# Optimization experiments

Measured on AMD Instinct MI355X. Metric: run time of the kernel, lower is better.

## Reference

```python
import jax, jax.numpy as jnp
import numpy as np

N = 100000
E = 1600000
IN_DIM = 128
OUT_DIM = 128


def setup_inputs() -> dict:
    key = jax.random.key(0)
    k1, k2, k3, k4, k5 = jax.random.split(key, 5)
    x = jax.random.normal(k1, (N, IN_DIM), dtype=jnp.float32)
    edge_index = jax.random.randint(k2, (2, E), 0, N, dtype=jnp.int64)
    # LayerNorm affine params
    ln_w = jnp.ones((IN_DIM,), dtype=jnp.float32)
    ln_b = jnp.zeros((IN_DIM,), dtype=jnp.float32)
    # SAGEConv params: lin_l (neighbor agg, with bias), lin_r (root, no bias)
    s = 1.0 / np.sqrt(IN_DIM)
    W_l = jax.random.uniform(k3, (OUT_DIM, IN_DIM), dtype=jnp.float32, minval=-s, maxval=s)
    b_l = jax.random.uniform(k4, (OUT_DIM,), dtype=jnp.float32, minval=-s, maxval=s)
    W_r = jax.random.uniform(k5, (OUT_DIM, IN_DIM), dtype=jnp.float32, minval=-s, maxval=s)
    return {"x": x, "edge_index": edge_index, "ln_w": ln_w, "ln_b": ln_b,
            "W_l": W_l, "b_l": b_l, "W_r": W_r}


def _layer_norm(x, w, b, eps=1e-5):
    mu = jnp.mean(x, axis=-1, keepdims=True)
    var = jnp.mean(jnp.square(x - mu), axis=-1, keepdims=True)
    return (x - mu) * jax.lax.rsqrt(var + eps) * w + b


def reference(x, edge_index, ln_w, ln_b, W_l, b_l, W_r):
    # norm -> activation -> dropout(p=0, identity)
    h = jax.nn.relu(_layer_norm(x, ln_w, ln_b))  # [N, in_dim]
    src = edge_index[0]  # message sources (x_j)
    dst = edge_index[1]  # aggregation targets
    # mean aggregation of neighbor features onto target nodes
    agg = jax.ops.segment_sum(h[src], dst, num_segments=N)  # [N, in_dim]
    cnt = jax.ops.segment_sum(jnp.ones((E,), dtype=h.dtype), dst, num_segments=N)
    agg = agg / jnp.maximum(cnt, 1.0)[:, None]
    # SAGEConv: lin_l(agg) + lin_r(h)
    out = agg @ W_l.T + b_l + h @ W_r.T  # [N, out_dim]
    return out
```

## Files before the change

kernel.cpp:

```cpp
#include <hip/hip_runtime.h>

#define N_NODES 100000
#define E_EDGES 1600000
#define DIM     128

#define NB1     391
#define NBINS   512
#define NBH     (NBINS * NB1)
#define HS_BLOCKS 196

#define HB_OFF    0
#define AGGB_OFF  25600000
#define WTB_OFF   51200000
#define OFFS_OFF  51265536
#define BH_OFF    51665600
#define BSUM_OFF  52468416
#define BIN_OFF   52469440

typedef __attribute__((ext_vector_type(8))) short short8;
typedef __attribute__((ext_vector_type(4))) float floatx4;

__device__ __forceinline__ unsigned bf16pack(float a, float b) {
  unsigned ua = __float_as_uint(a); ua += 0x7fffu + ((ua >> 16) & 1u);
  unsigned ub = __float_as_uint(b); ub += 0x7fffu + ((ub >> 16) & 1u);
  return (ua >> 16) | (ub & 0xffff0000u);
}
__device__ __forceinline__ float2 bf16unpack(unsigned p) {
  return make_float2(__uint_as_float(p << 16), __uint_as_float(p & 0xffff0000u));
}

__global__ __launch_bounds__(256) void k_prep(const float* __restrict__ x,
                                              const float* __restrict__ lw,
                                              const float* __restrict__ lb,
                                              const float* __restrict__ Wl,
                                              const float* __restrict__ Wr,
                                              unsigned* __restrict__ hb,
                                              unsigned* __restrict__ wtb) {
  int gid = blockIdx.x * 256 + threadIdx.x;

  {
    int row  = blockIdx.x * 4 + (threadIdx.x >> 6);
    int lane = threadIdx.x & 63;
    float2 v = ((const float2*)(x + (size_t)row * DIM))[lane];
    float s  = v.x + v.y;
    float sq = v.x * v.x + v.y * v.y;
    #pragma unroll
    for (int off = 32; off > 0; off >>= 1) {
      s  += __shfl_xor(s, off);
      sq += __shfl_xor(sq, off);
    }
    float mu  = s * (1.0f / 128.0f);
    float var = sq * (1.0f / 128.0f) - mu * mu;
    float rs  = rsqrtf(var + 1e-5f);
    float2 w = ((const float2*)lw)[lane];
    float2 b = ((const float2*)lb)[lane];
    float ox = fmaxf((v.x - mu) * rs * w.x + b.x, 0.0f);
    float oy = fmaxf((v.y - mu) * rs * w.y + b.y, 0.0f);
    hb[(size_t)row * 64 + lane] = bf16pack(ox, oy);
  }

  if (gid < 16384) {
    int j2 = gid & 3;
    int q  = (gid >> 2) & 3;
    int c  = (gid >> 4) & 127;
    int kb = gid >> 11;
    int k0 = kb * 32 + q * 8 + j2 * 2;
    int k1 = k0 + 1;
    float v0 = (k0 < 128) ? Wl[c * 128 + k0] : Wr[c * 128 + (k0 - 128)];
    float v1 = (k1 < 128) ? Wl[c * 128 + k1] : Wr[c * 128 + (k1 - 128)];
    wtb[gid] = bf16pack(v0, v1);
  }
}

__global__ __launch_bounds__(256) void k_hist1(const int* __restrict__ ei,
                                               int* __restrict__ bh) {
  __shared__ int h[NBINS];
  int t = threadIdx.x;
  h[t] = 0; h[t + 256] = 0;
  __syncthreads();
  const int4* d4p = (const int4*)(ei + E_EDGES);
  #pragma unroll
  for (int u = 0; u < 4; ++u) {
    int i4 = blockIdx.x * 1024 + u * 256 + t;
    if (i4 < E_EDGES / 4) {
      int4 d = d4p[i4];
      atomicAdd(&h[d.x >> 8], 1);
      atomicAdd(&h[d.y >> 8], 1);
      atomicAdd(&h[d.z >> 8], 1);
      atomicAdd(&h[d.w >> 8], 1);
    }
  }
  __syncthreads();
  bh[t * NB1 + blockIdx.x] = h[t];
  bh[(t + 256) * NB1 + blockIdx.x] = h[t + 256];
}

__global__ __launch_bounds__(256) void k_hscan1(int* __restrict__ bh,
                                                int* __restrict__ bsum) {
  __shared__ int s[256];
  int t = threadIdx.x;
  int base = blockIdx.x * 1024 + t * 4;
  int a0 = (base + 0 < NBH) ? bh[base + 0] : 0;
  int a1 = (base + 1 < NBH) ? bh[base + 1] : 0;
  int a2 = (base + 2 < NBH) ? bh[base + 2] : 0;
  int a3 = (base + 3 < NBH) ? bh[base + 3] : 0;
  s[t] = a0 + a1 + a2 + a3;
  __syncthreads();
  #pragma unroll
  for (int off = 1; off < 256; off <<= 1) {
    int x = (t >= off) ? s[t - off] : 0;
    __syncthreads();
    s[t] += x;
    __syncthreads();
  }
  int excl = (t > 0) ? s[t - 1] : 0;
  if (t == 255) bsum[blockIdx.x] = s[255];
  if (base + 0 < NBH) bh[base + 0] = excl;
  if (base + 1 < NBH) bh[base + 1] = excl + a0;
  if (base + 2 < NBH) bh[base + 2] = excl + a0 + a1;
  if (base + 3 < NBH) bh[base + 3] = excl + a0 + a1 + a2;
}

__global__ __launch_bounds__(256) void k_hscan2(int* __restrict__ bh,
                                                const int* __restrict__ bsum) {
  __shared__ int s[256];
  int t = threadIdx.x;
  s[t] = (t < HS_BLOCKS) ? bsum[t] : 0;
  __syncthreads();
  #pragma unroll
  for (int off = 1; off < 256; off <<= 1) {
    int x = (t >= off) ? s[t - off] : 0;
    __syncthreads();
    s[t] += x;
    __syncthreads();
  }
  int blk = blockIdx.x;
  int add = (blk > 0) ? s[blk - 1] : 0;
  #pragma unroll
  for (int u = 0; u < 4; ++u) {
    int i = blk * 1024 + t * 4 + u;
    if (i < NBH) bh[i] += add;
  }
}

__global__ __launch_bounds__(256) void k_scatter1(const int* __restrict__ ei,
                                                  const int* __restrict__ bh,
                                                  int* __restrict__ binned) {
  __shared__ int cur[NBINS];
  int t = threadIdx.x;
  cur[t] = bh[t * NB1 + blockIdx.x];
  cur[t + 256] = bh[(t + 256) * NB1 + blockIdx.x];
  __syncthreads();
  const int4* s4p = (const int4*)ei;
  const int4* d4p = (const int4*)(ei + E_EDGES);
  #pragma unroll
  for (int u = 0; u < 4; ++u) {
    int i4 = blockIdx.x * 1024 + u * 256 + t;
    if (i4 < E_EDGES / 4) {
      int4 sv = s4p[i4];
      int4 dv = d4p[i4];
      int p0 = atomicAdd(&cur[dv.x >> 8], 1);
      int p1 = atomicAdd(&cur[dv.y >> 8], 1);
      int p2 = atomicAdd(&cur[dv.z >> 8], 1);
      int p3 = atomicAdd(&cur[dv.w >> 8], 1);
      binned[p0] = sv.x | ((dv.x & 255) << 20);
      binned[p1] = sv.y | ((dv.y & 255) << 20);
      binned[p2] = sv.z | ((dv.z & 255) << 20);
      binned[p3] = sv.w | ((dv.w & 255) << 20);
    }
  }
}

__global__ __launch_bounds__(256) void k_csr(const int* __restrict__ bh,
                                             const int* __restrict__ binned,
                                             int* __restrict__ offs,
                                             int* __restrict__ srcidx) {
  __shared__ int h[256];
  __shared__ int s[256];
  __shared__ int cur[256];
  int t = threadIdx.x;
  int bin = blockIdx.x;
  int base = bh[bin * NB1];
  int end  = bh[(bin + 1) * NB1];
  h[t] = 0;
  __syncthreads();
  for (int i = base + t; i < end; i += 256)
    atomicAdd(&h[(binned[i] >> 20) & 255], 1);
  __syncthreads();
  s[t] = h[t];
  __syncthreads();
  #pragma unroll
  for (int off = 1; off < 256; off <<= 1) {
    int x = (t >= off) ? s[t - off] : 0;
    __syncthreads();
    s[t] += x;
    __syncthreads();
  }
  int excl = (t > 0) ? s[t - 1] : 0;
  cur[t] = excl;
  int node = bin * 256 + t;
  if (node < N_NODES) offs[node] = base + excl;
  if (node == N_NODES) offs[N_NODES] = E_EDGES;
  __syncthreads();
  for (int i = base + t; i < end; i += 256) {
    int p = binned[i];
    int r = atomicAdd(&cur[(p >> 20) & 255], 1);
    srcidx[base + r] = p & 0xFFFFF;
  }
}

__global__ __launch_bounds__(256) void k_gather(const unsigned* __restrict__ hb,
                                                const int* __restrict__ offs,
                                                const int* __restrict__ srcidx,
                                                unsigned* __restrict__ aggb) {
  int wave = threadIdx.x >> 6;
  int lane = threadIdx.x & 63;
  int n0 = blockIdx.x * 8 + wave * 2;
  int n1 = n0 + 1;
  int b0 = __builtin_amdgcn_readfirstlane(offs[n0]);
  int e0 = __builtin_amdgcn_readfirstlane(offs[n0 + 1]);
  int b1 = __builtin_amdgcn_readfirstlane(offs[n1]);
  int e1 = __builtin_amdgcn_readfirstlane(offs[n1 + 1]);
  int m0 = e0 - b0, m1 = e1 - b1;
  int c  = (m0 < m1 ? m0 : m1) & ~7;

  float ax0 = 0.0f, ay0 = 0.0f, ax1 = 0.0f, ay1 = 0.0f;

  for (int j = 0; j < c; j += 8) {
    unsigned p0[8], p1[8];
    #pragma unroll
    for (int i = 0; i < 8; ++i) {
      int s0 = srcidx[b0 + j + i];
      int s1 = srcidx[b1 + j + i];
      p0[i] = hb[(size_t)s0 * 64 + lane];
      p1[i] = hb[(size_t)s1 * 64 + lane];
    }
    #pragma unroll
    for (int i = 0; i < 8; ++i) {
      float2 v0 = bf16unpack(p0[i]);
      float2 v1 = bf16unpack(p1[i]);
      ax0 += v0.x; ay0 += v0.y;
      ax1 += v1.x; ay1 += v1.y;
    }
  }
  for (int j = b0 + c; j < e0; ) {
    int rem = e0 - j;
    if (rem >= 8) {
      unsigned p[8];
      #pragma unroll
      for (int i = 0; i < 8; ++i) p[i] = hb[(size_t)srcidx[j + i] * 64 + lane];
      #pragma unroll
      for (int i = 0; i < 8; ++i) { float2 v = bf16unpack(p[i]); ax0 += v.x; ay0 += v.y; }
      j += 8;
    } else {
      float2 v = bf16unpack(hb[(size_t)srcidx[j] * 64 + lane]);
      ax0 += v.x; ay0 += v.y;
      ++j;
    }
  }
  for (int j = b1 + c; j < e1; ) {
    int rem = e1 - j;
    if (rem >= 8) {
      unsigned p[8];
      #pragma unroll
      for (int i = 0; i < 8; ++i) p[i] = hb[(size_t)srcidx[j + i] * 64 + lane];
      #pragma unroll
      for (int i = 0; i < 8; ++i) { float2 v = bf16unpack(p[i]); ax1 += v.x; ay1 += v.y; }
      j += 8;
    } else {
      float2 v = bf16unpack(hb[(size_t)srcidx[j] * 64 + lane]);
      ax1 += v.x; ay1 += v.y;
      ++j;
    }
  }

  float inv0 = 1.0f / fmaxf((float)m0, 1.0f);
  float inv1 = 1.0f / fmaxf((float)m1, 1.0f);
  aggb[(size_t)n0 * 64 + lane] = bf16pack(ax0 * inv0, ay0 * inv0);
  aggb[(size_t)n1 * 64 + lane] = bf16pack(ax1 * inv1, ay1 * inv1);
}

__global__ __launch_bounds__(256) void k_gemm(const unsigned* __restrict__ aggb,
                                              const unsigned* __restrict__ hb,
                                              const unsigned* __restrict__ wtb,
                                              const float* __restrict__ bl,
                                              float* __restrict__ out) {
  int wave = threadIdx.x >> 6;
  int lane = threadIdx.x & 63;
  int m = lane & 15;
  int q = lane >> 4;
  int r0 = blockIdx.x * 64 + wave * 16;
  int rowA = r0 + m;
  if (rowA > N_NODES - 1) rowA = N_NODES - 1;

  const uint4* ar = (const uint4*)(aggb + (size_t)rowA * 64);
  const uint4* hr = (const uint4*)(hb + (size_t)rowA * 64);
  short8 afrag[8];
  #pragma unroll
  for (int kb = 0; kb < 4; ++kb) {
    uint4 u = ar[kb * 4 + q];
    afrag[kb] = *(short8*)&u;
  }
  #pragma unroll
  for (int kb = 0; kb < 4; ++kb) {
    uint4 u = hr[kb * 4 + q];
    afrag[kb + 4] = *(short8*)&u;
  }

  const uint4* b4 = (const uint4*)wtb;
  #pragma unroll
  for (int ct = 0; ct < 8; ++ct) {
    int c = ct * 16 + m;
    floatx4 acc = {0.0f, 0.0f, 0.0f, 0.0f};
    #pragma unroll
    for (int kb = 0; kb < 8; ++kb) {
      uint4 u = b4[kb * 512 + c * 4 + q];
      short8 bfrag = *(short8*)&u;
      acc = __builtin_amdgcn_mfma_f32_16x16x32_bf16(afrag[kb], bfrag, acc, 0, 0, 0);
    }
    float bias = bl[c];
    #pragma unroll
    for (int reg = 0; reg < 4; ++reg) {
      int r = r0 + q * 4 + reg;
      if (r < N_NODES) out[(size_t)r * DIM + c] = acc[reg] + bias;
    }
  }
}

extern "C" void kernel_launch(void* const* d_in, const int* in_sizes, int n_in,
                              void* d_out, int out_size, void* d_ws, size_t ws_size,
                              hipStream_t stream) {
  const float* x  = (const float*)d_in[0];
  const int*   ei = (const int*)d_in[1];
  const float* lw = (const float*)d_in[2];
  const float* lb = (const float*)d_in[3];
  const float* Wl = (const float*)d_in[4];
  const float* bl = (const float*)d_in[5];
  const float* Wr = (const float*)d_in[6];
  float* out = (float*)d_out;

  char* ws = (char*)d_ws;
  unsigned* hb     = (unsigned*)(ws + HB_OFF);
  unsigned* aggb   = (unsigned*)(ws + AGGB_OFF);
  unsigned* wtb    = (unsigned*)(ws + WTB_OFF);
  int*      offs   = (int*)(ws + OFFS_OFF);
  int*      bh     = (int*)(ws + BH_OFF);
  int*      bsum   = (int*)(ws + BSUM_OFF);
  int*      binned = (int*)(ws + BIN_OFF);
  int*      srcidx = binned;
  srcidx = (int*)(ws + BIN_OFF);

  srcidx = (int*)(ws + BIN_OFF + (size_t)E_EDGES * 4);

  k_prep<<<N_NODES / 4, 256, 0, stream>>>(x, lw, lb, Wl, Wr, hb, wtb);
  k_hist1<<<NB1, 256, 0, stream>>>(ei, bh);
  k_hscan1<<<HS_BLOCKS, 256, 0, stream>>>(bh, bsum);
  k_hscan2<<<HS_BLOCKS, 256, 0, stream>>>(bh, bsum);
  k_scatter1<<<NB1, 256, 0, stream>>>(ei, bh, binned);
  k_csr<<<NB1, 256, 0, stream>>>(bh, binned, offs, srcidx);
  k_gather<<<N_NODES / 8, 256, 0, stream>>>(hb, offs, srcidx, aggb);
  k_gemm<<<(N_NODES + 63) / 64, 256, 0, stream>>>(aggb, hb, wtb, bl, out);
}
```

Baseline: 265.8 us.

## Fuse all stages into one persistent cooperative kernel with grid syncs

Replaces the eight separate kernel launches with a single persistent cooperative kernel. Its blocks grid-stride over each former stage, and grid.sync() separates the stages. This removes per-launch overhead and inter-kernel gaps. In exchange, occupancy is capped by the cooperative grid size and launch bounds, the whole grid waits at every barrier, and large stages like the gather now run with fewer resident blocks.

```diff
diff --git a/kernel.cpp b/kernel.cpp
--- a/kernel.cpp
+++ b/kernel.cpp
@@ -1,4 +1,7 @@
 #include <hip/hip_runtime.h>
+#include <hip/hip_cooperative_groups.h>
+
+namespace cg = cooperative_groups;
 
 #define N_NODES 100000
 #define E_EDGES 1600000
@@ -16,6 +19,7 @@
 #define BH_OFF    51665600
 #define BSUM_OFF  52468416
 #define BIN_OFF   52469440
+#define SRC_OFF   58869440
 
 typedef __attribute__((ext_vector_type(8))) short short8;
 typedef __attribute__((ext_vector_type(4))) float floatx4;
@@ -29,28 +33,41 @@
   return make_float2(__uint_as_float(p << 16), __uint_as_float(p & 0xffff0000u));
 }
 
-__global__ __launch_bounds__(256) void k_prep(const float* __restrict__ x,
-                                              const float* __restrict__ lw,
-                                              const float* __restrict__ lb,
-                                              const float* __restrict__ Wl,
-                                              const float* __restrict__ Wr,
-                                              unsigned* __restrict__ hb,
-                                              unsigned* __restrict__ wtb) {
-  int gid = blockIdx.x * 256 + threadIdx.x;
-
-  {
-    int row  = blockIdx.x * 4 + (threadIdx.x >> 6);
-    int lane = threadIdx.x & 63;
+__global__ __launch_bounds__(256, 4) void k_mega(
+    const float* __restrict__ x, const int* __restrict__ ei,
+    const float* __restrict__ lw, const float* __restrict__ lb,
+    const float* __restrict__ Wl, const float* __restrict__ bl,
+    const float* __restrict__ Wr, float* __restrict__ out,
+    char* __restrict__ ws) {
+  unsigned* hb     = (unsigned*)(ws + HB_OFF);
+  unsigned* aggb   = (unsigned*)(ws + AGGB_OFF);
+  unsigned* wtb    = (unsigned*)(ws + WTB_OFF);
+  int*      offs   = (int*)(ws + OFFS_OFF);
+  int*      bh     = (int*)(ws + BH_OFF);
+  int*      bsum   = (int*)(ws + BSUM_OFF);
+  int*      binned = (int*)(ws + BIN_OFF);
+  int*      srcidx = (int*)(ws + SRC_OFF);
+
+  cg::grid_group grid = cg::this_grid();
+  __shared__ int smem[768];
+  const int t    = threadIdx.x;
+  const int blk  = blockIdx.x;
+  const int gdim = gridDim.x;
+  const int lane = t & 63;
+  const int wv   = t >> 6;
+
+  for (int g = blk; g < N_NODES / 4; g += gdim) {
+    int row = g * 4 + wv;
     float2 v = ((const float2*)(x + (size_t)row * DIM))[lane];
-    float s  = v.x + v.y;
-    float sq = v.x * v.x + v.y * v.y;
+    float sAcc = v.x + v.y;
+    float qAcc = v.x * v.x + v.y * v.y;
     #pragma unroll
     for (int off = 32; off > 0; off >>= 1) {
-      s  += __shfl_xor(s, off);
-      sq += __shfl_xor(sq, off);
-    }
-    float mu  = s * (1.0f / 128.0f);
-    float var = sq * (1.0f / 128.0f) - mu * mu;
+      sAcc += __shfl_xor(sAcc, off);
+      qAcc += __shfl_xor(qAcc, off);
+    }
+    float mu  = sAcc * (1.0f / 128.0f);
+    float var = qAcc * (1.0f / 128.0f) - mu * mu;
     float rs  = rsqrtf(var + 1e-5f);
     float2 w = ((const float2*)lw)[lane];
     float2 b = ((const float2*)lb)[lane];
@@ -58,271 +75,251 @@
     float oy = fmaxf((v.y - mu) * rs * w.y + b.y, 0.0f);
     hb[(size_t)row * 64 + lane] = bf16pack(ox, oy);
   }
-
-  if (gid < 16384) {
-    int j2 = gid & 3;
-    int q  = (gid >> 2) & 3;
-    int c  = (gid >> 4) & 127;
-    int kb = gid >> 11;
-    int k0 = kb * 32 + q * 8 + j2 * 2;
-    int k1 = k0 + 1;
-    float v0 = (k0 < 128) ? Wl[c * 128 + k0] : Wr[c * 128 + (k0 - 128)];
-    float v1 = (k1 < 128) ? Wl[c * 128 + k1] : Wr[c * 128 + (k1 - 128)];
-    wtb[gid] = bf16pack(v0, v1);
-  }
-}
-
-__global__ __launch_bounds__(256) void k_hist1(const int* __restrict__ ei,
-                                               int* __restrict__ bh) {
-  __shared__ int h[NBINS];
-  int t = threadIdx.x;
-  h[t] = 0; h[t + 256] = 0;
-  __syncthreads();
-  const int4* d4p = (const int4*)(ei + E_EDGES);
-  #pragma unroll
-  for (int u = 0; u < 4; ++u) {
-    int i4 = blockIdx.x * 1024 + u * 256 + t;
-    if (i4 < E_EDGES / 4) {
-      int4 d = d4p[i4];
-      atomicAdd(&h[d.x >> 8], 1);
-      atomicAdd(&h[d.y >> 8], 1);
-      atomicAdd(&h[d.z >> 8], 1);
-      atomicAdd(&h[d.w >> 8], 1);
-    }
-  }
-  __syncthreads();
-  bh[t * NB1 + blockIdx.x] = h[t];
-  bh[(t + 256) * NB1 + blockIdx.x] = h[t + 256];
-}
-
-__global__ __launch_bounds__(256) void k_hscan1(int* __restrict__ bh,
-                                                int* __restrict__ bsum) {
-  __shared__ int s[256];
-  int t = threadIdx.x;
-  int base = blockIdx.x * 1024 + t * 4;
-  int a0 = (base + 0 < NBH) ? bh[base + 0] : 0;
-  int a1 = (base + 1 < NBH) ? bh[base + 1] : 0;
-  int a2 = (base + 2 < NBH) ? bh[base + 2] : 0;
-  int a3 = (base + 3 < NBH) ? bh[base + 3] : 0;
-  s[t] = a0 + a1 + a2 + a3;
-  __syncthreads();
-  #pragma unroll
-  for (int off = 1; off < 256; off <<= 1) {
-    int x = (t >= off) ? s[t - off] : 0;
-    __syncthreads();
-    s[t] += x;
-    __syncthreads();
-  }
-  int excl = (t > 0) ? s[t - 1] : 0;
-  if (t == 255) bsum[blockIdx.x] = s[255];
-  if (base + 0 < NBH) bh[base + 0] = excl;
-  if (base + 1 < NBH) bh[base + 1] = excl + a0;
-  if (base + 2 < NBH) bh[base + 2] = excl + a0 + a1;
-  if (base + 3 < NBH) bh[base + 3] = excl + a0 + a1 + a2;
-}
-
-__global__ __launch_bounds__(256) void k_hscan2(int* __restrict__ bh,
-                                                const int* __restrict__ bsum) {
-  __shared__ int s[256];
-  int t = threadIdx.x;
-  s[t] = (t < HS_BLOCKS) ? bsum[t] : 0;
-  __syncthreads();
-  #pragma unroll
-  for (int off = 1; off < 256; off <<= 1) {
-    int x = (t >= off) ? s[t - off] : 0;
-    __syncthreads();
-    s[t] += x;
-    __syncthreads();
-  }
-  int blk = blockIdx.x;
-  int add = (blk > 0) ? s[blk - 1] : 0;
-  #pragma unroll
-  for (int u = 0; u < 4; ++u) {
-    int i = blk * 1024 + t * 4 + u;
-    if (i < NBH) bh[i] += add;
-  }
-}
-
-__global__ __launch_bounds__(256) void k_scatter1(const int* __restrict__ ei,
-                                                  const int* __restrict__ bh,
-                                                  int* __restrict__ binned) {
-  __shared__ int cur[NBINS];
-  int t = threadIdx.x;
-  cur[t] = bh[t * NB1 + blockIdx.x];
-  cur[t + 256] = bh[(t + 256) * NB1 + blockIdx.x];
-  __syncthreads();
-  const int4* s4p = (const int4*)ei;
-  const int4* d4p = (const int4*)(ei + E_EDGES);
-  #pragma unroll
-  for (int u = 0; u < 4; ++u) {
-    int i4 = blockIdx.x * 1024 + u * 256 + t;
-    if (i4 < E_EDGES / 4) {
-      int4 sv = s4p[i4];
-      int4 dv = d4p[i4];
-      int p0 = atomicAdd(&cur[dv.x >> 8], 1);
-      int p1 = atomicAdd(&cur[dv.y >> 8], 1);
-      int p2 = atomicAdd(&cur[dv.z >> 8], 1);
-      int p3 = atomicAdd(&cur[dv.w >> 8], 1);
-      binned[p0] = sv.x | ((dv.x & 255) << 20);
-      binned[p1] = sv.y | ((dv.y & 255) << 20);
-      binned[p2] = sv.z | ((dv.z & 255) << 20);
-      binned[p3] = sv.w | ((dv.w & 255) << 20);
-    }
-  }
-}
-
-__global__ __launch_bounds__(256) void k_csr(const int* __restrict__ bh,
-                                             const int* __restrict__ binned,
-                                             int* __restrict__ offs,
-                                             int* __restrict__ srcidx) {
-  __shared__ int h[256];
-  __shared__ int s[256];
-  __shared__ int cur[256];
-  int t = threadIdx.x;
-  int bin = blockIdx.x;
-  int base = bh[bin * NB1];
-  int end  = bh[(bin + 1) * NB1];
-  h[t] = 0;
-  __syncthreads();
-  for (int i = base + t; i < end; i += 256)
-    atomicAdd(&h[(binned[i] >> 20) & 255], 1);
-  __syncthreads();
-  s[t] = h[t];
-  __syncthreads();
-  #pragma unroll
-  for (int off = 1; off < 256; off <<= 1) {
-    int x = (t >= off) ? s[t - off] : 0;
-    __syncthreads();
-    s[t] += x;
-    __syncthreads();
-  }
-  int excl = (t > 0) ? s[t - 1] : 0;
-  cur[t] = excl;
-  int node = bin * 256 + t;
-  if (node < N_NODES) offs[node] = base + excl;
-  if (node == N_NODES) offs[N_NODES] = E_EDGES;
-  __syncthreads();
-  for (int i = base + t; i < end; i += 256) {
-    int p = binned[i];
-    int r = atomicAdd(&cur[(p >> 20) & 255], 1);
-    srcidx[base + r] = p & 0xFFFFF;
-  }
-}
-
-__global__ __launch_bounds__(256) void k_gather(const unsigned* __restrict__ hb,
-                                                const int* __restrict__ offs,
-                                                const int* __restrict__ srcidx,
-                                                unsigned* __restrict__ aggb) {
-  int wave = threadIdx.x >> 6;
-  int lane = threadIdx.x & 63;
-  int n0 = blockIdx.x * 8 + wave * 2;
-  int n1 = n0 + 1;
-  int b0 = __builtin_amdgcn_readfirstlane(offs[n0]);
-  int e0 = __builtin_amdgcn_readfirstlane(offs[n0 + 1]);
-  int b1 = __builtin_amdgcn_readfirstlane(offs[n1]);
-  int e1 = __builtin_amdgcn_readfirstlane(offs[n1 + 1]);
-  int m0 = e0 - b0, m1 = e1 - b1;
-  int c  = (m0 < m1 ? m0 : m1) & ~7;
-
-  float ax0 = 0.0f, ay0 = 0.0f, ax1 = 0.0f, ay1 = 0.0f;
-
-  for (int j = 0; j < c; j += 8) {
-    unsigned p0[8], p1[8];
-    #pragma unroll
-    for (int i = 0; i < 8; ++i) {
-      int s0 = srcidx[b0 + j + i];
-      int s1 = srcidx[b1 + j + i];
-      p0[i] = hb[(size_t)s0 * 64 + lane];
-      p1[i] = hb[(size_t)s1 * 64 + lane];
-    }
-    #pragma unroll
-    for (int i = 0; i < 8; ++i) {
-      float2 v0 = bf16unpack(p0[i]);
-      float2 v1 = bf16unpack(p1[i]);
-      ax0 += v0.x; ay0 += v0.y;
-      ax1 += v1.x; ay1 += v1.y;
-    }
-  }
-  for (int j = b0 + c; j < e0; ) {
-    int rem = e0 - j;
-    if (rem >= 8) {
-      unsigned p[8];
+  {
+    int gid = blk * 256 + t;
+    if (gid < 16384) {
+      int j2 = gid & 3;
+      int q  = (gid >> 2) & 3;
+      int c  = (gid >> 4) & 127;
+      int kb = gid >> 11;
+      int k0 = kb * 32 + q * 8 + j2 * 2;
+      int k1 = k0 + 1;
+      float v0 = (k0 < 128) ? Wl[c * 128 + k0] : Wr[c * 128 + (k0 - 128)];
+      float v1 = (k1 < 128) ? Wl[c * 128 + k1] : Wr[c * 128 + (k1 - 128)];
+      wtb[gid] = bf16pack(v0, v1);
+    }
+  }
+  for (int ch = blk; ch < NB1; ch += gdim) {
+    smem[t] = 0; smem[t + 256] = 0;
+    __syncthreads();
+    const int4* d4p = (const int4*)(ei + E_EDGES);
+    #pragma unroll
+    for (int u = 0; u < 4; ++u) {
+      int i4 = ch * 1024 + u * 256 + t;
+      if (i4 < E_EDGES / 4) {
+        int4 d = d4p[i4];
+        atomicAdd(&smem[d.x >> 8], 1);
+        atomicAdd(&smem[d.y >> 8], 1);
+        atomicAdd(&smem[d.z >> 8], 1);
+        atomicAdd(&smem[d.w >> 8], 1);
+      }
+    }
+    __syncthreads();
+    bh[t * NB1 + ch] = smem[t];
+    bh[(t + 256) * NB1 + ch] = smem[t + 256];
+    __syncthreads();
+  }
+  grid.sync();
+
+  if (blk < HS_BLOCKS) {
+    int base = blk * 1024 + t * 4;
+    int a0 = (base + 0 < NBH) ? bh[base + 0] : 0;
+    int a1 = (base + 1 < NBH) ? bh[base + 1] : 0;
+    int a2 = (base + 2 < NBH) ? bh[base + 2] : 0;
+    int a3 = (base + 3 < NBH) ? bh[base + 3] : 0;
+    smem[t] = a0 + a1 + a2 + a3;
+    __syncthreads();
+    #pragma unroll
+    for (int off = 1; off < 256; off <<= 1) {
+      int xv = (t >= off) ? smem[t - off] : 0;
+      __syncthreads();
+      smem[t] += xv;
+      __syncthreads();
+    }
+    int excl = (t > 0) ? smem[t - 1] : 0;
+    if (t == 255) bsum[blk] = smem[255];
+    if (base + 0 < NBH) bh[base + 0] = excl;
+    if (base + 1 < NBH) bh[base + 1] = excl + a0;
+    if (base + 2 < NBH) bh[base + 2] = excl + a0 + a1;
+    if (base + 3 < NBH) bh[base + 3] = excl + a0 + a1 + a2;
+  }
+  grid.sync();
+
+  if (blk < HS_BLOCKS) {
+    smem[t] = (t < HS_BLOCKS) ? bsum[t] : 0;
+    __syncthreads();
+    #pragma unroll
+    for (int off = 1; off < 256; off <<= 1) {
+      int xv = (t >= off) ? smem[t - off] : 0;
+      __syncthreads();
+      smem[t] += xv;
+      __syncthreads();
+    }
+    int add = (blk > 0) ? smem[blk - 1] : 0;
+    #pragma unroll
+    for (int u = 0; u < 4; ++u) {
+      int i = blk * 1024 + t * 4 + u;
+      if (i < NBH) bh[i] += add;
+    }
+  }
+  grid.sync();
+
+  for (int ch = blk; ch < NB1; ch += gdim) {
+    smem[t] = bh[t * NB1 + ch];
+    smem[t + 256] = bh[(t + 256) * NB1 + ch];
+    __syncthreads();
+    const int4* s4p = (const int4*)ei;
+    const int4* d4p = (const int4*)(ei + E_EDGES);
+    #pragma unroll
+    for (int u = 0; u < 4; ++u) {
+      int i4 = ch * 1024 + u * 256 + t;
+      if (i4 < E_EDGES / 4) {
+        int4 sv = s4p[i4];
+        int4 dv = d4p[i4];
+        int p0 = atomicAdd(&smem[dv.x >> 8], 1);
+        int p1 = atomicAdd(&smem[dv.y >> 8], 1);
+        int p2 = atomicAdd(&smem[dv.z >> 8], 1);
+        int p3 = atomicAdd(&smem[dv.w >> 8], 1);
+        binned[p0] = sv.x | ((dv.x & 255) << 20);
+        binned[p1] = sv.y | ((dv.y & 255) << 20);
+        binned[p2] = sv.z | ((dv.z & 255) << 20);
+        binned[p3] = sv.w | ((dv.w & 255) << 20);
+      }
+    }
+    __syncthreads();
+  }
+  grid.sync();
+
+  for (int bin = blk; bin < NB1; bin += gdim) {
+    int* h   = smem;
+    int* sc  = smem + 256;
+    int* cur = smem + 512;
+    int base = bh[bin * NB1];
+    int end  = bh[(bin + 1) * NB1];
+    h[t] = 0;
+    __syncthreads();
+    for (int i = base + t; i < end; i += 256)
+      atomicAdd(&h[(binned[i] >> 20) & 255], 1);
+    __syncthreads();
+    sc[t] = h[t];
+    __syncthreads();
+    #pragma unroll
+    for (int off = 1; off < 256; off <<= 1) {
+      int xv = (t >= off) ? sc[t - off] : 0;
+      __syncthreads();
+      sc[t] += xv;
+      __syncthreads();
+    }
+    int excl = (t > 0) ? sc[t - 1] : 0;
+    cur[t] = excl;
+    int node = bin * 256 + t;
+    if (node < N_NODES) offs[node] = base + excl;
+    if (node == N_NODES) offs[N_NODES] = E_EDGES;
+    __syncthreads();
+    for (int i = base + t; i < end; i += 256) {
+      int p = binned[i];
+      int r = atomicAdd(&cur[(p >> 20) & 255], 1);
+      srcidx[base + r] = p & 0xFFFFF;
+    }
+    __syncthreads();
+  }
+  grid.sync();
+
+  for (int g = blk; g < N_NODES / 8; g += gdim) {
+    int n0 = g * 8 + wv * 2;
+    int n1 = n0 + 1;
+    int b0 = __builtin_amdgcn_readfirstlane(offs[n0]);
+    int e0 = __builtin_amdgcn_readfirstlane(offs[n0 + 1]);
+    int b1 = __builtin_amdgcn_readfirstlane(offs[n1]);
+    int e1 = __builtin_amdgcn_readfirstlane(offs[n1 + 1]);
+    int m0 = e0 - b0, m1 = e1 - b1;
+    int c  = (m0 < m1 ? m0 : m1) & ~7;
+
+    float ax0 = 0.0f, ay0 = 0.0f, ax1 = 0.0f, ay1 = 0.0f;
+
+    for (int j = 0; j < c; j += 8) {
+      unsigned p0[8], p1[8];
       #pragma unroll
-      for (int i = 0; i < 8; ++i) p[i] = hb[(size_t)srcidx[j + i] * 64 + lane];
+      for (int i = 0; i < 8; ++i) {
+        int s0 = srcidx[b0 + j + i];
+        int s1 = srcidx[b1 + j + i];
+        p0[i] = hb[(size_t)s0 * 64 + lane];
+        p1[i] = hb[(size_t)s1 * 64 + lane];
+      }
       #pragma unroll
-      for (int i = 0; i < 8; ++i) { float2 v = bf16unpack(p[i]); ax0 += v.x; ay0 += v.y; }
-      j += 8;
-    } else {
-      float2 v = bf16unpack(hb[(size_t)srcidx[j] * 64 + lane]);
-      ax0 += v.x; ay0 += v.y;
-      ++j;
-    }
-  }
-  for (int j = b1 + c; j < e1; ) {
-    int rem = e1 - j;
-    if (rem >= 8) {
-      unsigned p[8];
+      for (int i = 0; i < 8; ++i) {
+        float2 v0 = bf16unpack(p0[i]);
+        float2 v1 = bf16unpack(p1[i]);
+        ax0 += v0.x; ay0 += v0.y;
+        ax1 += v1.x; ay1 += v1.y;
+      }
+    }
+    for (int j = b0 + c; j < e0; ) {
+      int rem = e0 - j;
+      if (rem >= 8) {
+        unsigned p[8];
+        #pragma unroll
+        for (int i = 0; i < 8; ++i) p[i] = hb[(size_t)srcidx[j + i] * 64 + lane];
+        #pragma unroll
+        for (int i = 0; i < 8; ++i) { float2 v = bf16unpack(p[i]); ax0 += v.x; ay0 += v.y; }
+        j += 8;
+      } else {
+        float2 v = bf16unpack(hb[(size_t)srcidx[j] * 64 + lane]);
+        ax0 += v.x; ay0 += v.y;
+        ++j;
+      }
+    }
+    for (int j = b1 + c; j < e1; ) {
+      int rem = e1 - j;
+      if (rem >= 8) {
+        unsigned p[8];
+        #pragma unroll
+        for (int i = 0; i < 8; ++i) p[i] = hb[(size_t)srcidx[j + i] * 64 + lane];
+        #pragma unroll
+        for (int i = 0; i < 8; ++i) { float2 v = bf16unpack(p[i]); ax1 += v.x; ay1 += v.y; }
+        j += 8;
+      } else {
+        float2 v = bf16unpack(hb[(size_t)srcidx[j] * 64 + lane]);
+        ax1 += v.x; ay1 += v.y;
+        ++j;
+      }
+    }
+
+    float inv0 = 1.0f / fmaxf((float)m0, 1.0f);
+    float inv1 = 1.0f / fmaxf((float)m1, 1.0f);
+    aggb[(size_t)n0 * 64 + lane] = bf16pack(ax0 * inv0, ay0 * inv0);
+    aggb[(size_t)n1 * 64 + lane] = bf16pack(ax1 * inv1, ay1 * inv1);
+  }
+  grid.sync();
+
+  for (int g = blk; g < (N_NODES + 63) / 64; g += gdim) {
+    int m = lane & 15;
+    int q = lane >> 4;
+    int r0 = g * 64 + wv * 16;
+    int rowA = r0 + m;
+    if (rowA > N_NODES - 1) rowA = N_NODES - 1;
+
+    const uint4* ar = (const uint4*)(aggb + (size_t)rowA * 64);
+    const uint4* hr = (const uint4*)(hb + (size_t)rowA * 64);
+    short8 afrag[8];
+    #pragma unroll
+    for (int kb = 0; kb < 4; ++kb) {
+      uint4 u = ar[kb * 4 + q];
+      afrag[kb] = *(short8*)&u;
+    }
+    #pragma unroll
+    for (int kb = 0; kb < 4; ++kb) {
+      uint4 u = hr[kb * 4 + q];
+      afrag[kb + 4] = *(short8*)&u;
+    }
+
+    const uint4* b4 = (const uint4*)wtb;
+    #pragma unroll
+    for (int ct = 0; ct < 8; ++ct) {
+      int c = ct * 16 + m;
+      floatx4 acc = {0.0f, 0.0f, 0.0f, 0.0f};
       #pragma unroll
-      for (int i = 0; i < 8; ++i) p[i] = hb[(size_t)srcidx[j + i] * 64 + lane];
+      for (int kb = 0; kb < 8; ++kb) {
+        uint4 u = b4[kb * 512 + c * 4 + q];
+        short8 bfrag = *(short8*)&u;
+        acc = __builtin_amdgcn_mfma_f32_16x16x32_bf16(afrag[kb], bfrag, acc, 0, 0, 0);
+      }
+      float bias = bl[c];
       #pragma unroll
-      for (int i = 0; i < 8; ++i) { float2 v = bf16unpack(p[i]); ax1 += v.x; ay1 += v.y; }
-      j += 8;
-    } else {
-      float2 v = bf16unpack(hb[(size_t)srcidx[j] * 64 + lane]);
-      ax1 += v.x; ay1 += v.y;
-      ++j;
-    }
-  }
-
-  float inv0 = 1.0f / fmaxf((float)m0, 1.0f);
-  float inv1 = 1.0f / fmaxf((float)m1, 1.0f);
-  aggb[(size_t)n0 * 64 + lane] = bf16pack(ax0 * inv0, ay0 * inv0);
-  aggb[(size_t)n1 * 64 + lane] = bf16pack(ax1 * inv1, ay1 * inv1);
-}
-
-__global__ __launch_bounds__(256) void k_gemm(const unsigned* __restrict__ aggb,
-                                              const unsigned* __restrict__ hb,
-                                              const unsigned* __restrict__ wtb,
-                                              const float* __restrict__ bl,
-                                              float* __restrict__ out) {
-  int wave = threadIdx.x >> 6;
-  int lane = threadIdx.x & 63;
-  int m = lane & 15;
-  int q = lane >> 4;
-  int r0 = blockIdx.x * 64 + wave * 16;
-  int rowA = r0 + m;
-  if (rowA > N_NODES - 1) rowA = N_NODES - 1;
-
-  const uint4* ar = (const uint4*)(aggb + (size_t)rowA * 64);
-  const uint4* hr = (const uint4*)(hb + (size_t)rowA * 64);
-  short8 afrag[8];
-  #pragma unroll
-  for (int kb = 0; kb < 4; ++kb) {
-    uint4 u = ar[kb * 4 + q];
-    afrag[kb] = *(short8*)&u;
-  }
-  #pragma unroll
-  for (int kb = 0; kb < 4; ++kb) {
-    uint4 u = hr[kb * 4 + q];
-    afrag[kb + 4] = *(short8*)&u;
-  }
-
-  const uint4* b4 = (const uint4*)wtb;
-  #pragma unroll
-  for (int ct = 0; ct < 8; ++ct) {
-    int c = ct * 16 + m;
-    floatx4 acc = {0.0f, 0.0f, 0.0f, 0.0f};
-    #pragma unroll
-    for (int kb = 0; kb < 8; ++kb) {
-      uint4 u = b4[kb * 512 + c * 4 + q];
-      short8 bfrag = *(short8*)&u;
-      acc = __builtin_amdgcn_mfma_f32_16x16x32_bf16(afrag[kb], bfrag, acc, 0, 0, 0);
-    }
-    float bias = bl[c];
-    #pragma unroll
-    for (int reg = 0; reg < 4; ++reg) {
-      int r = r0 + q * 4 + reg;
-      if (r < N_NODES) out[(size_t)r * DIM + c] = acc[reg] + bias;
+      for (int reg = 0; reg < 4; ++reg) {
+        int r = r0 + q * 4 + reg;
+        if (r < N_NODES) out[(size_t)r * DIM + c] = acc[reg] + bias;
+      }
     }
   }
 }
@@ -338,26 +335,20 @@
   const float* bl = (const float*)d_in[5];
   const float* Wr = (const float*)d_in[6];
   float* out = (float*)d_out;
-
   char* ws = (char*)d_ws;
-  unsigned* hb     = (unsigned*)(ws + HB_OFF);
-  unsigned* aggb   = (unsigned*)(ws + AGGB_OFF);
-  unsigned* wtb    = (unsigned*)(ws + WTB_OFF);
-  int*      offs   = (int*)(ws + OFFS_OFF);
-  int*      bh     = (int*)(ws + BH_OFF);
-  int*      bsum   = (int*)(ws + BSUM_OFF);
-  int*      binned = (int*)(ws + BIN_OFF);
-  int*      srcidx = binned;
-  srcidx = (int*)(ws + BIN_OFF);
-
-  srcidx = (int*)(ws + BIN_OFF + (size_t)E_EDGES * 4);
-
-  k_prep<<<N_NODES / 4, 256, 0, stream>>>(x, lw, lb, Wl, Wr, hb, wtb);
-  k_hist1<<<NB1, 256, 0, stream>>>(ei, bh);
-  k_hscan1<<<HS_BLOCKS, 256, 0, stream>>>(bh, bsum);
-  k_hscan2<<<HS_BLOCKS, 256, 0, stream>>>(bh, bsum);
-  k_scatter1<<<NB1, 256, 0, stream>>>(ei, bh, binned);
-  k_csr<<<NB1, 256, 0, stream>>>(bh, binned, offs, srcidx);
-  k_gather<<<N_NODES / 8, 256, 0, stream>>>(hb, offs, srcidx, aggb);
-  k_gemm<<<(N_NODES + 63) / 64, 256, 0, stream>>>(aggb, hb, wtb, bl, out);
+
+  static int grid = 0;
+  if (grid == 0) {
+    int maxB = 0;
+    (void)hipOccupancyMaxActiveBlocksPerMultiprocessor(&maxB, k_mega, 256, 0);
+    if (maxB < 1) maxB = 1;
+    grid = 256 * maxB;
+    if (grid > 1024) grid = 1024;
+  }
+
+  void* args[9];
+  args[0] = (void*)&x;  args[1] = (void*)&ei; args[2] = (void*)&lw;
+  args[3] = (void*)&lb; args[4] = (void*)&Wl; args[5] = (void*)&bl;
+  args[6] = (void*)&Wr; args[7] = (void*)&out; args[8] = (void*)&ws;
+  hipLaunchCooperativeKernel((void*)k_mega, dim3(grid), dim3(256), args, 0, stream);
 }
```

New measurement: 834.5 us. +214.0%, slower.

## Fuse gather and GEMM via shared-memory aggregate tile; fold histogram into prep

Applied to the files above, without the earlier changes.

The neighbor-mean gather and the bf16 MFMA GEMM become a single kernel. Each 512-thread block aggregates 16 nodes into an LDS tile, and each of its 8 waves computes one 16-column output slice. This drops the round trip of the aggregate buffer through global memory and removes a launch. The edge histogram kernel is also merged into the prep kernel's first blocks to save another launch. In exchange, the weight fragments are reloaded per 16-row tile, and blocks are larger with a barrier between the gather and GEMM phases.

```diff
diff --git a/kernel.cpp b/kernel.cpp
--- a/kernel.cpp
+++ b/kernel.cpp
@@ -10,12 +10,12 @@
 #define HS_BLOCKS 196
 
 #define HB_OFF    0
-#define AGGB_OFF  25600000
-#define WTB_OFF   51200000
-#define OFFS_OFF  51265536
-#define BH_OFF    51665600
-#define BSUM_OFF  52468416
-#define BIN_OFF   52469440
+#define WTB_OFF   25600000
+#define OFFS_OFF  25665536
+#define BH_OFF    26065600
+#define BSUM_OFF  26868416
+#define BIN_OFF   26869440
+#define SRC_OFF   33269440
 
 typedef __attribute__((ext_vector_type(8))) short short8;
 typedef __attribute__((ext_vector_type(4))) float floatx4;
@@ -34,13 +34,16 @@
                                               const float* __restrict__ lb,
                                               const float* __restrict__ Wl,
                                               const float* __restrict__ Wr,
+                                              const int* __restrict__ ei,
                                               unsigned* __restrict__ hb,
-                                              unsigned* __restrict__ wtb) {
+                                              unsigned* __restrict__ wtb,
+                                              int* __restrict__ bh) {
   int gid = blockIdx.x * 256 + threadIdx.x;
+  int t = threadIdx.x;
 
   {
-    int row  = blockIdx.x * 4 + (threadIdx.x >> 6);
-    int lane = threadIdx.x & 63;
+    int row  = blockIdx.x * 4 + (t >> 6);
+    int lane = t & 63;
     float2 v = ((const float2*)(x + (size_t)row * DIM))[lane];
     float s  = v.x + v.y;
     float sq = v.x * v.x + v.y * v.y;
@@ -70,29 +73,27 @@
     float v1 = (k1 < 128) ? Wl[c * 128 + k1] : Wr[c * 128 + (k1 - 128)];
     wtb[gid] = bf16pack(v0, v1);
   }
-}
-
-__global__ __launch_bounds__(256) void k_hist1(const int* __restrict__ ei,
-                                               int* __restrict__ bh) {
-  __shared__ int h[NBINS];
-  int t = threadIdx.x;
-  h[t] = 0; h[t + 256] = 0;
-  __syncthreads();
-  const int4* d4p = (const int4*)(ei + E_EDGES);
-  #pragma unroll
-  for (int u = 0; u < 4; ++u) {
-    int i4 = blockIdx.x * 1024 + u * 256 + t;
-    if (i4 < E_EDGES / 4) {
-      int4 d = d4p[i4];
-      atomicAdd(&h[d.x >> 8], 1);
-      atomicAdd(&h[d.y >> 8], 1);
-      atomicAdd(&h[d.z >> 8], 1);
-      atomicAdd(&h[d.w >> 8], 1);
-    }
-  }
-  __syncthreads();
-  bh[t * NB1 + blockIdx.x] = h[t];
-  bh[(t + 256) * NB1 + blockIdx.x] = h[t + 256];
+
+  if (blockIdx.x < NB1) {
+    __shared__ int h[NBINS];
+    h[t] = 0; h[t + 256] = 0;
+    __syncthreads();
+    const int4* d4p = (const int4*)(ei + E_EDGES);
+    #pragma unroll
+    for (int u = 0; u < 4; ++u) {
+      int i4 = blockIdx.x * 1024 + u * 256 + t;
+      if (i4 < E_EDGES / 4) {
+        int4 d = d4p[i4];
+        atomicAdd(&h[d.x >> 8], 1);
+        atomicAdd(&h[d.y >> 8], 1);
+        atomicAdd(&h[d.z >> 8], 1);
+        atomicAdd(&h[d.w >> 8], 1);
+      }
+    }
+    __syncthreads();
+    bh[t * NB1 + blockIdx.x] = h[t];
+    bh[(t + 256) * NB1 + blockIdx.x] = h[t + 256];
+  }
 }
 
 __global__ __launch_bounds__(256) void k_hscan1(int* __restrict__ bh,
@@ -209,13 +210,17 @@
   }
 }
 
-__global__ __launch_bounds__(256) void k_gather(const unsigned* __restrict__ hb,
-                                                const int* __restrict__ offs,
-                                                const int* __restrict__ srcidx,
-                                                unsigned* __restrict__ aggb) {
-  int wave = threadIdx.x >> 6;
+__global__ __launch_bounds__(512) void k_gathgemm(const unsigned* __restrict__ hb,
+                                                  const int* __restrict__ offs,
+                                                  const int* __restrict__ srcidx,
+                                                  const unsigned* __restrict__ wtb,
+                                                  const float* __restrict__ bl,
+                                                  float* __restrict__ out) {
+  __shared__ unsigned agg[16 * 68];
+  int wv   = threadIdx.x >> 6;
   int lane = threadIdx.x & 63;
-  int n0 = blockIdx.x * 8 + wave * 2;
+  int r0 = blockIdx.x * 16;
+  int n0 = r0 + wv * 2;
   int n1 = n0 + 1;
   int b0 = __builtin_amdgcn_readfirstlane(offs[n0]);
   int e0 = __builtin_amdgcn_readfirstlane(offs[n0 + 1]);
@@ -276,31 +281,21 @@
 
   float inv0 = 1.0f / fmaxf((float)m0, 1.0f);
   float inv1 = 1.0f / fmaxf((float)m1, 1.0f);
-  aggb[(size_t)n0 * 64 + lane] = bf16pack(ax0 * inv0, ay0 * inv0);
-  aggb[(size_t)n1 * 64 + lane] = bf16pack(ax1 * inv1, ay1 * inv1);
-}
-
-__global__ __launch_bounds__(256) void k_gemm(const unsigned* __restrict__ aggb,
-                                              const unsigned* __restrict__ hb,
-                                              const unsigned* __restrict__ wtb,
-                                              const float* __restrict__ bl,
-                                              float* __restrict__ out) {
-  int wave = threadIdx.x >> 6;
-  int lane = threadIdx.x & 63;
+  agg[(wv * 2 + 0) * 68 + lane] = bf16pack(ax0 * inv0, ay0 * inv0);
+  agg[(wv * 2 + 1) * 68 + lane] = bf16pack(ax1 * inv1, ay1 * inv1);
+  __syncthreads();
+
   int m = lane & 15;
   int q = lane >> 4;
-  int r0 = blockIdx.x * 64 + wave * 16;
   int rowA = r0 + m;
-  if (rowA > N_NODES - 1) rowA = N_NODES - 1;
-
-  const uint4* ar = (const uint4*)(aggb + (size_t)rowA * 64);
+
+  short8 afrag[8];
+  #pragma unroll
+  for (int kb = 0; kb < 4; ++kb) {
+    uint4 u = *(const uint4*)&agg[m * 68 + (kb * 4 + q) * 4];
+    afrag[kb] = *(short8*)&u;
+  }
   const uint4* hr = (const uint4*)(hb + (size_t)rowA * 64);
-  short8 afrag[8];
-  #pragma unroll
-  for (int kb = 0; kb < 4; ++kb) {
-    uint4 u = ar[kb * 4 + q];
-    afrag[kb] = *(short8*)&u;
-  }
   #pragma unroll
   for (int kb = 0; kb < 4; ++kb) {
     uint4 u = hr[kb * 4 + q];
@@ -308,22 +303,20 @@
   }
 
   const uint4* b4 = (const uint4*)wtb;
-  #pragma unroll
-  for (int ct = 0; ct < 8; ++ct) {
-    int c = ct * 16 + m;
-    floatx4 acc = {0.0f, 0.0f, 0.0f, 0.0f};
-    #pragma unroll
-    for (int kb = 0; kb < 8; ++kb) {
-      uint4 u = b4[kb * 512 + c * 4 + q];
-      short8 bfrag = *(short8*)&u;
-      acc = __builtin_amdgcn_mfma_f32_16x16x32_bf16(afrag[kb], bfrag, acc, 0, 0, 0);
-    }
-    float bias = bl[c];
-    #pragma unroll
-    for (int reg = 0; reg < 4; ++reg) {
-      int r = r0 + q * 4 + reg;
-      if (r < N_NODES) out[(size_t)r * DIM + c] = acc[reg] + bias;
-    }
+  int ct = wv;
+  int col = ct * 16 + m;
+  floatx4 acc = {0.0f, 0.0f, 0.0f, 0.0f};
+  #pragma unroll
+  for (int kb = 0; kb < 8; ++kb) {
+    uint4 u = b4[kb * 512 + col * 4 + q];
+    short8 bfrag = *(short8*)&u;
+    acc = __builtin_amdgcn_mfma_f32_16x16x32_bf16(afrag[kb], bfrag, acc, 0, 0, 0);
+  }
+  float bias = bl[col];
+  #pragma unroll
+  for (int reg = 0; reg < 4; ++reg) {
+    int r = r0 + q * 4 + reg;
+    out[(size_t)r * DIM + col] = acc[reg] + bias;
   }
 }
 
@@ -341,23 +334,17 @@
 
   char* ws = (char*)d_ws;
   unsigned* hb     = (unsigned*)(ws + HB_OFF);
-  unsigned* aggb   = (unsigned*)(ws + AGGB_OFF);
   unsigned* wtb    = (unsigned*)(ws + WTB_OFF);
   int*      offs   = (int*)(ws + OFFS_OFF);
   int*      bh     = (int*)(ws + BH_OFF);
   int*      bsum   = (int*)(ws + BSUM_OFF);
   int*      binned = (int*)(ws + BIN_OFF);
-  int*      srcidx = binned;
-  srcidx = (int*)(ws + BIN_OFF);
-
-  srcidx = (int*)(ws + BIN_OFF + (size_t)E_EDGES * 4);
-
-  k_prep<<<N_NODES / 4, 256, 0, stream>>>(x, lw, lb, Wl, Wr, hb, wtb);
-  k_hist1<<<NB1, 256, 0, stream>>>(ei, bh);
+  int*      srcidx = (int*)(ws + SRC_OFF);
+
+  k_prep<<<N_NODES / 4, 256, 0, stream>>>(x, lw, lb, Wl, Wr, ei, hb, wtb, bh);
   k_hscan1<<<HS_BLOCKS, 256, 0, stream>>>(bh, bsum);
   k_hscan2<<<HS_BLOCKS, 256, 0, stream>>>(bh, bsum);
   k_scatter1<<<NB1, 256, 0, stream>>>(ei, bh, binned);
   k_csr<<<NB1, 256, 0, stream>>>(bh, binned, offs, srcidx);
-  k_gather<<<N_NODES / 8, 256, 0, stream>>>(hb, offs, srcidx, aggb);
-  k_gemm<<<(N_NODES + 63) / 64, 256, 0, stream>>>(aggb, hb, wtb, bl, out);
-}
+  k_gathgemm<<<N_NODES / 16, 512, 0, stream>>>(hb, offs, srcidx, wtb, bl, out);
+}
```

After: 261.7 us. Within noise of the previous version (-1.5%).
